# Performance work log

Measured on AMD Instinct MI355X. Metric: run time of the kernel, lower is better.

Reference implementation:

```python
import jax, jax.numpy as jnp
import numpy as np

DIM_K = 128
MODEL_DIM = 1024
B, S = 8, 2048

def setup_inputs() -> dict:
    key = jax.random.key(0)
    k1, k2, k3, k4, k5, k6, k7 = jax.random.split(key, 7)
    return {
        "query": jax.random.normal(k1, (B, S, MODEL_DIM), dtype=jnp.float32),
        "key": jax.random.normal(k2, (B, S, MODEL_DIM), dtype=jnp.float32),
        "value": jax.random.normal(k3, (B, S, MODEL_DIM), dtype=jnp.float32),
        "mask": jax.random.randint(k4, (B, S, S), 0, 2, dtype=jnp.int32),
        # nn.Linear(model_dim, dim_k, bias=False): weight shape [dim_k, model_dim]
        "Wq": jax.random.normal(k5, (DIM_K, MODEL_DIM), dtype=jnp.float32) * (MODEL_DIM ** -0.5),
        "Wk": jax.random.normal(k6, (DIM_K, MODEL_DIM), dtype=jnp.float32) * (MODEL_DIM ** -0.5),
        "Wv": jax.random.normal(k7, (DIM_K, MODEL_DIM), dtype=jnp.float32) * (MODEL_DIM ** -0.5),
    }

def reference(query, key, value, mask, Wq, Wk, Wv):
    # projections: y = x @ W.T
    q = jnp.einsum('bsm,km->bsk', query, Wq)
    k = jnp.einsum('bsm,km->bsk', key, Wk)
    v = jnp.einsum('bsm,km->bsk', value, Wv)
    scale = 1.0 / jnp.sqrt(jnp.float32(DIM_K))
    pre_score = jnp.einsum('bqk,bsk->bqs', q, k) * scale  # [B,Sq,Sk]
    pre_score = jnp.where(mask == 0, jnp.float32(-1e9), pre_score)
    score = jax.nn.softmax(pre_score, axis=-1)
    return jnp.einsum('bqs,bsk->bqk', score, v)
```

## Files before the change

kernel.cpp:

```cpp
#include <hip/hip_runtime.h>
#include <hip/hip_bf16.h>

#define SEQ 2048
#define DMODEL 1024
#define DK 128

typedef __bf16 bf16x8 __attribute__((ext_vector_type(8)));
typedef float  f32x4  __attribute__((ext_vector_type(4)));

#define L2E 1.44269504088896340736f

#define WS_Q  786432
#define WS_K  2883584
#define WS_VT 4980736
#define WS_BF16_BYTES 14155776ull

__global__ __launch_bounds__(256) void wconv_kernel(
    const float* __restrict__ wq, const float* __restrict__ wk,
    const float* __restrict__ wv, __bf16* __restrict__ wpack)
{
    int i = blockIdx.x * 256 + threadIdx.x;
    int p = i >> 17;
    int j = i & 131071;
    const float* src = (p == 0) ? wq : ((p == 1) ? wk : wv);
    float f = src[j];
    if (p == 0) f *= 0.08838834764831845f;
    __bf16 h = (__bf16)f;
    __bf16 l = (__bf16)(f - (float)h);
    wpack[p * 262144 + j]          = h;
    wpack[p * 262144 + 131072 + j] = l;
}

__global__ __launch_bounds__(256) void proj_kernel(
    const float* __restrict__ xq, const float* __restrict__ xk,
    const float* __restrict__ xv, const __bf16* __restrict__ wpack,
    __bf16* __restrict__ qws, __bf16* __restrict__ kws, __bf16* __restrict__ vtws)
{
    const int p = blockIdx.y;
    const float* __restrict__ x = (p == 0) ? xq : ((p == 1) ? xk : xv);
    const __bf16* __restrict__ whi_g = wpack + p * 262144;
    const __bf16* __restrict__ wlo_g = whi_g + 131072;

    const int mtile = blockIdx.x;
    const int m0 = mtile << 6;
    const int t = threadIdx.x;
    const int wv_ = t >> 6;
    const int lane = t & 63;
    const int l15 = lane & 15, g = lane >> 4;

    __shared__ __align__(16) __bf16 smem[18432];
    __bf16* whl = smem;
    __bf16* wll = smem + 9216;

    f32x4 acc[8];
#pragma unroll
    for (int nt = 0; nt < 8; ++nt) acc[nt] = (f32x4){0.f, 0.f, 0.f, 0.f};

    for (int kk = 0; kk < 16; ++kk) {
        __syncthreads();
#pragma unroll
        for (int i = 0; i < 8; ++i) {
            int idx = i * 256 + t;
            int h = idx >> 10, rem = idx & 1023;
            int row = rem >> 3, ck = rem & 7;
            const __bf16* src = (h ? wlo_g : whi_g) + row * 1024 + kk * 64 + ck * 8;
            __bf16* dst = (h ? wll : whl) + row * 72 + ck * 8;
            *(bf16x8*)dst = *(const bf16x8*)src;
        }
        __syncthreads();

#pragma unroll
        for (int ks = 0; ks < 2; ++ks) {
            int row = m0 + wv_ * 16 + l15;
            int col = kk * 64 + ks * 32 + g * 8;
            const float* xp = x + (size_t)row * 1024 + col;
            f32x4 a0 = *(const f32x4*)xp;
            f32x4 a1 = *(const f32x4*)(xp + 4);
            bf16x8 ah;
#pragma unroll
            for (int j = 0; j < 4; ++j) {
                ah[j] = (__bf16)a0[j];
                ah[4 + j] = (__bf16)a1[j];
            }
#pragma unroll
            for (int nt = 0; nt < 8; ++nt) {
                const __bf16* bp = whl + (nt * 16 + l15) * 72 + ks * 32 + g * 8;
                bf16x8 bh = *(const bf16x8*)bp;
                bf16x8 bl = *(const bf16x8*)(bp + 9216);
                acc[nt] = __builtin_amdgcn_mfma_f32_16x16x32_bf16(ah, bh, acc[nt], 0, 0, 0);
                acc[nt] = __builtin_amdgcn_mfma_f32_16x16x32_bf16(ah, bl, acc[nt], 0, 0, 0);
            }
        }
    }

    __syncthreads();
    __bf16* olds = smem;
#pragma unroll
    for (int nt = 0; nt < 8; ++nt)
#pragma unroll
        for (int r = 0; r < 4; ++r) {
            int rowl = wv_ * 16 + g * 4 + r;
            int col = nt * 16 + l15;
            __bf16 v = (__bf16)acc[nt][r];
            if (p < 2) olds[rowl * 136 + col] = v;
            else       olds[col * 72 + rowl] = v;
        }
    __syncthreads();

    const int bq = mtile >> 5, s0 = (mtile & 31) << 6;
    if (p < 2) {
#pragma unroll
        for (int i = 0; i < 4; ++i) {
            int idx = i * 256 + t;
            int row = idx >> 4, ck = idx & 15;
            bf16x8 v = *(const bf16x8*)(olds + row * 136 + ck * 8);
            __bf16* dst = ((p == 0) ? qws : kws) + (size_t)(m0 + row) * 128 + ck * 8;
            *(bf16x8*)dst = v;
        }
    } else {
#pragma unroll
        for (int i = 0; i < 4; ++i) {
            int idx = i * 256 + t;
            int row = idx >> 3, ck = idx & 7;
            bf16x8 v = *(const bf16x8*)(olds + row * 72 + ck * 8);
            __bf16* dst = vtws + ((size_t)(bq * 128 + row)) * 2048 + s0 + ck * 8;
            *(bf16x8*)dst = v;
        }
    }
}

__global__ __launch_bounds__(256) void flash_kernel(
    const __bf16* __restrict__ qws, const __bf16* __restrict__ kws,
    const __bf16* __restrict__ vtws, const int* __restrict__ mask,
    float* __restrict__ out, float* __restrict__ part, float* __restrict__ mlbuf,
    int ktp)
{
    const int bb = blockIdx.x & 7;
    const int rest = blockIdx.x >> 3;
    const int mtile = rest & 31;
    const int jsplit = rest >> 5;
    const int sq0 = mtile << 6;
    const int t = threadIdx.x;
    const int wv_ = t >> 6;
    const int lane = t & 63;
    const int l15 = lane & 15, g = lane >> 4;

    __shared__ __align__(16) __bf16 smem[22528];
    __bf16* klds = smem;
    __bf16* vtlds = smem + 8704;
    __bf16* plds = smem + 17920 + wv_ * 1152;

    bf16x8 qf[4];
    {
        const __bf16* qp = qws + ((size_t)(bb * 2048 + sq0 + wv_ * 16 + l15)) * 128 + g * 8;
#pragma unroll
        for (int ks = 0; ks < 4; ++ks) qf[ks] = *(const bf16x8*)(qp + ks * 32);
    }

    f32x4 o[8];
#pragma unroll
    for (int nt = 0; nt < 8; ++nt) o[nt] = (f32x4){0.f, 0.f, 0.f, 0.f};
    float m_run[4], l_run[4];
#pragma unroll
    for (int r = 0; r < 4; ++r) { m_run[r] = -__builtin_inff(); l_run[r] = 0.f; }

    const int* mbase = mask + ((size_t)(bb * 2048 + sq0 + wv_ * 16 + g * 4)) * 2048 + l15;

    const int kt_begin = jsplit * ktp, kt_end = kt_begin + ktp;
    for (int kt = kt_begin; kt < kt_end; ++kt) {
        const int n0 = kt << 6;
        __syncthreads();
#pragma unroll
        for (int i = 0; i < 8; ++i) {
            int idx = i * 256 + t;
            if (idx < 1024) {
                int row = idx >> 4, ck = idx & 15;
                *(bf16x8*)(klds + row * 136 + ck * 8) =
                    *(const bf16x8*)(kws + ((size_t)(bb * 2048 + n0 + row)) * 128 + ck * 8);
            } else {
                int v = idx - 1024;
                int row = v >> 3, ck = v & 7;
                *(bf16x8*)(vtlds + row * 72 + ck * 8) =
                    *(const bf16x8*)(vtws + ((size_t)(bb * 128 + row)) * 2048 + n0 + ck * 8);
            }
        }
        __syncthreads();

        int mv[4][4];
#pragma unroll
        for (int nt = 0; nt < 4; ++nt)
#pragma unroll
            for (int r = 0; r < 4; ++r)
                mv[nt][r] = mbase[(size_t)r * 2048 + n0 + nt * 16];

        f32x4 sf[4];
#pragma unroll
        for (int nt = 0; nt < 4; ++nt) sf[nt] = (f32x4){0.f, 0.f, 0.f, 0.f};
#pragma unroll
        for (int nt = 0; nt < 4; ++nt) {
            const __bf16* kp = klds + (nt * 16 + l15) * 136 + g * 8;
#pragma unroll
            for (int ks = 0; ks < 4; ++ks) {
                bf16x8 bfk = *(const bf16x8*)(kp + ks * 32);
                sf[nt] = __builtin_amdgcn_mfma_f32_16x16x32_bf16(qf[ks], bfk, sf[nt], 0, 0, 0);
            }
        }

        float mx[4], mnew[4], alpha[4], psum[4];
#pragma unroll
        for (int r = 0; r < 4; ++r)
            mx[r] = fmaxf(fmaxf(sf[0][r], sf[1][r]), fmaxf(sf[2][r], sf[3][r]));
#pragma unroll
        for (int off = 1; off < 16; off <<= 1)
#pragma unroll
            for (int r = 0; r < 4; ++r)
                mx[r] = fmaxf(mx[r], __shfl_xor(mx[r], off, 64));
#pragma unroll
        for (int r = 0; r < 4; ++r) {
            mnew[r] = fmaxf(m_run[r], mx[r]);
            alpha[r] = exp2f((m_run[r] - mnew[r]) * L2E);
            psum[r] = 0.f;
        }
#pragma unroll
        for (int nt = 0; nt < 4; ++nt)
#pragma unroll
            for (int r = 0; r < 4; ++r) {
                float pv = exp2f((sf[nt][r] - mnew[r]) * L2E);
                pv = mv[nt][r] ? pv : 0.f;
                psum[r] += pv;
                plds[(g * 4 + r) * 72 + nt * 16 + l15] = (__bf16)pv;
            }
#pragma unroll
        for (int off = 1; off < 16; off <<= 1)
#pragma unroll
            for (int r = 0; r < 4; ++r)
                psum[r] += __shfl_xor(psum[r], off, 64);
#pragma unroll
        for (int r = 0; r < 4; ++r) {
            l_run[r] = l_run[r] * alpha[r] + psum[r];
            m_run[r] = mnew[r];
        }
#pragma unroll
        for (int nt = 0; nt < 8; ++nt)
#pragma unroll
            for (int r = 0; r < 4; ++r) o[nt][r] *= alpha[r];

        bf16x8 pa[2];
#pragma unroll
        for (int ks2 = 0; ks2 < 2; ++ks2)
            pa[ks2] = *(const bf16x8*)(plds + l15 * 72 + ks2 * 32 + g * 8);

#pragma unroll
        for (int nt2 = 0; nt2 < 8; ++nt2) {
            const __bf16* vp = vtlds + (nt2 * 16 + l15) * 72 + g * 8;
#pragma unroll
            for (int ks2 = 0; ks2 < 2; ++ks2) {
                bf16x8 bfv = *(const bf16x8*)(vp + ks2 * 32);
                o[nt2] = __builtin_amdgcn_mfma_f32_16x16x32_bf16(pa[ks2], bfv, o[nt2], 0, 0, 0);
            }
        }
    }

    if (part == nullptr) {
        float inv[4];
#pragma unroll
        for (int r = 0; r < 4; ++r) inv[r] = 1.0f / l_run[r];
#pragma unroll
        for (int nt2 = 0; nt2 < 8; ++nt2)
#pragma unroll
            for (int r = 0; r < 4; ++r)
                out[((size_t)(bb * 2048 + sq0 + wv_ * 16 + g * 4 + r)) * 128 + nt2 * 16 + l15] =
                    o[nt2][r] * inv[r];
    } else {
#pragma unroll
        for (int nt2 = 0; nt2 < 8; ++nt2)
#pragma unroll
            for (int r = 0; r < 4; ++r) {
                size_t rowg = (size_t)(bb * 2048 + sq0 + wv_ * 16 + g * 4 + r);
                part[((size_t)jsplit * 16384 + rowg) * 128 + nt2 * 16 + l15] = o[nt2][r];
            }
        if (l15 == 0) {
#pragma unroll
            for (int r = 0; r < 4; ++r) {
                size_t rowg = (size_t)(bb * 2048 + sq0 + wv_ * 16 + g * 4 + r);
                mlbuf[((size_t)jsplit * 16384 + rowg) * 2]     = m_run[r];
                mlbuf[((size_t)jsplit * 16384 + rowg) * 2 + 1] = l_run[r];
            }
        }
    }
}

__global__ __launch_bounds__(256) void merge_kernel(
    const float* __restrict__ part, const float* __restrict__ mlbuf,
    float* __restrict__ out, int J)
{
    int t = threadIdx.x;
    size_t row = (size_t)blockIdx.x * 8 + (t >> 5);
    int c = (t & 31) * 4;
    float mj[4];
    float m = -__builtin_inff();
    for (int j = 0; j < J; ++j) {
        mj[j] = mlbuf[((size_t)j * 16384 + row) * 2];
        m = fmaxf(m, mj[j]);
    }
    float l = 0.f;
    f32x4 acc = (f32x4){0.f, 0.f, 0.f, 0.f};
    for (int j = 0; j < J; ++j) {
        float w = exp2f((mj[j] - m) * L2E);
        l += w * mlbuf[((size_t)j * 16384 + row) * 2 + 1];
        f32x4 v = *(const f32x4*)(part + ((size_t)j * 16384 + row) * 128 + c);
#pragma unroll
        for (int e = 0; e < 4; ++e) acc[e] += w * v[e];
    }
    float inv = 1.0f / l;
#pragma unroll
    for (int e = 0; e < 4; ++e) acc[e] *= inv;
    *(f32x4*)(out + row * 128 + c) = acc;
}

extern "C" void kernel_launch(void* const* d_in, const int* in_sizes, int n_in,
                              void* d_out, int out_size, void* d_ws, size_t ws_size,
                              hipStream_t stream)
{
    const float* query = (const float*)d_in[0];
    const float* key   = (const float*)d_in[1];
    const float* value = (const float*)d_in[2];
    const int*   mask  = (const int*)d_in[3];
    const float* Wq    = (const float*)d_in[4];
    const float* Wk    = (const float*)d_in[5];
    const float* Wv    = (const float*)d_in[6];
    float* out = (float*)d_out;

    __bf16* wpack = (__bf16*)d_ws;
    __bf16* qws = wpack + WS_Q;
    __bf16* kws = wpack + WS_K;
    __bf16* vtws = wpack + WS_VT;

    const size_t per_split = 16384ull * 128 * 4 + 16384ull * 8;
    int J = 1;
    if (ws_size >= WS_BF16_BYTES + 4 * per_split)      J = 4;
    else if (ws_size >= WS_BF16_BYTES + 2 * per_split) J = 2;
    float* part = (J > 1) ? (float*)((char*)d_ws + WS_BF16_BYTES) : nullptr;
    float* mlbuf = (J > 1) ? (part + (size_t)J * 16384 * 128) : nullptr;

    wconv_kernel<<<1536, 256, 0, stream>>>(Wq, Wk, Wv, wpack);
    proj_kernel<<<dim3(256, 3), 256, 0, stream>>>(query, key, value, wpack, qws, kws, vtws);
    flash_kernel<<<256 * J, 256, 0, stream>>>(qws, kws, vtws, mask, out, part, mlbuf, 32 / J);
    if (J > 1) merge_kernel<<<2048, 256, 0, stream>>>(part, mlbuf, out, J);
}
```

Baseline: 413.5 us.

## Switch to fp16 and restructure projection to read weights directly without LDS

Replaces bf16 with fp16 across the pipeline. This drops the hi/lo split-weight trick and halves the projection MFMAs. The projection kernel now uses 128 threads, each wave computing 32 rows, and reads fp16 weights straight from global/L2 instead of staging them through LDS with barriers. This removes the redundant second MFMA pass and the per-k-step synchronisation. The risk is fp16 range and precision limits on projected activations, plus higher global traffic for the weight reads.

```diff
diff --git a/kernel.cpp b/kernel.cpp
--- a/kernel.cpp
+++ b/kernel.cpp
@@ -1,23 +1,23 @@
 #include <hip/hip_runtime.h>
-#include <hip/hip_bf16.h>
+#include <hip/hip_fp16.h>
 
 #define SEQ 2048
 #define DMODEL 1024
 #define DK 128
 
-typedef __bf16 bf16x8 __attribute__((ext_vector_type(8)));
-typedef float  f32x4  __attribute__((ext_vector_type(4)));
+typedef _Float16 f16x8 __attribute__((ext_vector_type(8)));
+typedef float    f32x4 __attribute__((ext_vector_type(4)));
 
 #define L2E 1.44269504088896340736f
 
-#define WS_Q  786432
-#define WS_K  2883584
-#define WS_VT 4980736
-#define WS_BF16_BYTES 14155776ull
+#define WS_Q  393216
+#define WS_K  2490368
+#define WS_VT 4587520
+#define WS_F16_BYTES 13369344ull
 
 __global__ __launch_bounds__(256) void wconv_kernel(
     const float* __restrict__ wq, const float* __restrict__ wk,
-    const float* __restrict__ wv, __bf16* __restrict__ wpack)
+    const float* __restrict__ wv, _Float16* __restrict__ w16)
 {
     int i = blockIdx.x * 256 + threadIdx.x;
     int p = i >> 17;
@@ -25,21 +25,17 @@
     const float* src = (p == 0) ? wq : ((p == 1) ? wk : wv);
     float f = src[j];
     if (p == 0) f *= 0.08838834764831845f;
-    __bf16 h = (__bf16)f;
-    __bf16 l = (__bf16)(f - (float)h);
-    wpack[p * 262144 + j]          = h;
-    wpack[p * 262144 + 131072 + j] = l;
-}
-
-__global__ __launch_bounds__(256) void proj_kernel(
+    w16[i] = (_Float16)f;
+}
+
+__global__ __launch_bounds__(128) void proj_kernel(
     const float* __restrict__ xq, const float* __restrict__ xk,
-    const float* __restrict__ xv, const __bf16* __restrict__ wpack,
-    __bf16* __restrict__ qws, __bf16* __restrict__ kws, __bf16* __restrict__ vtws)
+    const float* __restrict__ xv, const _Float16* __restrict__ w16,
+    _Float16* __restrict__ qws, _Float16* __restrict__ kws, _Float16* __restrict__ vtws)
 {
     const int p = blockIdx.y;
     const float* __restrict__ x = (p == 0) ? xq : ((p == 1) ? xk : xv);
-    const __bf16* __restrict__ whi_g = wpack + p * 262144;
-    const __bf16* __restrict__ wlo_g = whi_g + 131072;
+    const _Float16* __restrict__ w = w16 + p * 131072;
 
     const int mtile = blockIdx.x;
     const int m0 = mtile << 6;
@@ -47,91 +43,81 @@
     const int wv_ = t >> 6;
     const int lane = t & 63;
     const int l15 = lane & 15, g = lane >> 4;
-
-    __shared__ __align__(16) __bf16 smem[18432];
-    __bf16* whl = smem;
-    __bf16* wll = smem + 9216;
-
-    f32x4 acc[8];
-#pragma unroll
-    for (int nt = 0; nt < 8; ++nt) acc[nt] = (f32x4){0.f, 0.f, 0.f, 0.f};
-
-    for (int kk = 0; kk < 16; ++kk) {
-        __syncthreads();
+    const int mw = m0 + wv_ * 32;
+
+    f32x4 acc[2][8];
+#pragma unroll
+    for (int mi = 0; mi < 2; ++mi)
+#pragma unroll
+        for (int nt = 0; nt < 8; ++nt) acc[mi][nt] = (f32x4){0.f, 0.f, 0.f, 0.f};
+
+    const float* x0 = x + (size_t)(mw + l15) * 1024 + g * 8;
+    const float* x1 = x0 + 16 * 1024;
+    const _Float16* wb = w + (size_t)l15 * 1024 + g * 8;
+
+#pragma unroll 2
+    for (int ks = 0; ks < 32; ++ks) {
+        const int col = ks * 32;
+        f32x4 a00 = *(const f32x4*)(x0 + col);
+        f32x4 a01 = *(const f32x4*)(x0 + col + 4);
+        f32x4 a10 = *(const f32x4*)(x1 + col);
+        f32x4 a11 = *(const f32x4*)(x1 + col + 4);
+        f16x8 af0, af1;
+#pragma unroll
+        for (int j = 0; j < 4; ++j) {
+            af0[j]     = (_Float16)a00[j];
+            af0[4 + j] = (_Float16)a01[j];
+            af1[j]     = (_Float16)a10[j];
+            af1[4 + j] = (_Float16)a11[j];
+        }
+#pragma unroll
+        for (int nt = 0; nt < 8; ++nt) {
+            f16x8 bf = *(const f16x8*)(wb + (size_t)nt * 16 * 1024 + col);
+            acc[0][nt] = __builtin_amdgcn_mfma_f32_16x16x32_f16(af0, bf, acc[0][nt], 0, 0, 0);
+            acc[1][nt] = __builtin_amdgcn_mfma_f32_16x16x32_f16(af1, bf, acc[1][nt], 0, 0, 0);
+        }
+    }
+
+    __shared__ __align__(16) _Float16 olds[9216];
+#pragma unroll
+    for (int mi = 0; mi < 2; ++mi)
+#pragma unroll
+        for (int nt = 0; nt < 8; ++nt)
+#pragma unroll
+            for (int r = 0; r < 4; ++r) {
+                int rowl = wv_ * 32 + mi * 16 + g * 4 + r;
+                int col = nt * 16 + l15;
+                _Float16 v = (_Float16)acc[mi][nt][r];
+                if (p < 2) olds[rowl * 136 + col] = v;
+                else       olds[col * 72 + rowl] = v;
+            }
+    __syncthreads();
+
+    if (p < 2) {
 #pragma unroll
         for (int i = 0; i < 8; ++i) {
-            int idx = i * 256 + t;
-            int h = idx >> 10, rem = idx & 1023;
-            int row = rem >> 3, ck = rem & 7;
-            const __bf16* src = (h ? wlo_g : whi_g) + row * 1024 + kk * 64 + ck * 8;
-            __bf16* dst = (h ? wll : whl) + row * 72 + ck * 8;
-            *(bf16x8*)dst = *(const bf16x8*)src;
-        }
-        __syncthreads();
-
-#pragma unroll
-        for (int ks = 0; ks < 2; ++ks) {
-            int row = m0 + wv_ * 16 + l15;
-            int col = kk * 64 + ks * 32 + g * 8;
-            const float* xp = x + (size_t)row * 1024 + col;
-            f32x4 a0 = *(const f32x4*)xp;
-            f32x4 a1 = *(const f32x4*)(xp + 4);
-            bf16x8 ah;
-#pragma unroll
-            for (int j = 0; j < 4; ++j) {
-                ah[j] = (__bf16)a0[j];
-                ah[4 + j] = (__bf16)a1[j];
-            }
-#pragma unroll
-            for (int nt = 0; nt < 8; ++nt) {
-                const __bf16* bp = whl + (nt * 16 + l15) * 72 + ks * 32 + g * 8;
-                bf16x8 bh = *(const bf16x8*)bp;
-                bf16x8 bl = *(const bf16x8*)(bp + 9216);
-                acc[nt] = __builtin_amdgcn_mfma_f32_16x16x32_bf16(ah, bh, acc[nt], 0, 0, 0);
-                acc[nt] = __builtin_amdgcn_mfma_f32_16x16x32_bf16(ah, bl, acc[nt], 0, 0, 0);
-            }
-        }
-    }
-
-    __syncthreads();
-    __bf16* olds = smem;
-#pragma unroll
-    for (int nt = 0; nt < 8; ++nt)
-#pragma unroll
-        for (int r = 0; r < 4; ++r) {
-            int rowl = wv_ * 16 + g * 4 + r;
-            int col = nt * 16 + l15;
-            __bf16 v = (__bf16)acc[nt][r];
-            if (p < 2) olds[rowl * 136 + col] = v;
-            else       olds[col * 72 + rowl] = v;
-        }
-    __syncthreads();
-
-    const int bq = mtile >> 5, s0 = (mtile & 31) << 6;
-    if (p < 2) {
-#pragma unroll
-        for (int i = 0; i < 4; ++i) {
-            int idx = i * 256 + t;
+            int idx = i * 128 + t;
             int row = idx >> 4, ck = idx & 15;
-            bf16x8 v = *(const bf16x8*)(olds + row * 136 + ck * 8);
-            __bf16* dst = ((p == 0) ? qws : kws) + (size_t)(m0 + row) * 128 + ck * 8;
-            *(bf16x8*)dst = v;
+            f16x8 v = *(const f16x8*)(olds + row * 136 + ck * 8);
+            _Float16* dst = ((p == 0) ? qws : kws) + (size_t)(m0 + row) * 128 + ck * 8;
+            *(f16x8*)dst = v;
         }
     } else {
-#pragma unroll
-        for (int i = 0; i < 4; ++i) {
-            int idx = i * 256 + t;
+        const int bq = mtile >> 5, s0 = (mtile & 31) << 6;
+#pragma unroll
+        for (int i = 0; i < 8; ++i) {
+            int idx = i * 128 + t;
             int row = idx >> 3, ck = idx & 7;
-            bf16x8 v = *(const bf16x8*)(olds + row * 72 + ck * 8);
-            __bf16* dst = vtws + ((size_t)(bq * 128 + row)) * 2048 + s0 + ck * 8;
-            *(bf16x8*)dst = v;
+            f16x8 v = *(const f16x8*)(olds + row * 72 + ck * 8);
+            _Float16* dst = vtws + ((size_t)(bq * 128 + row)) * 2048 + s0 + ck * 8;
+            *(f16x8*)dst = v;
         }
     }
 }
 
 __global__ __launch_bounds__(256) void flash_kernel(
-    const __bf16* __restrict__ qws, const __bf16* __restrict__ kws,
-    const __bf16* __restrict__ vtws, const int* __restrict__ mask,
+    const _Float16* __restrict__ qws, const _Float16* __restrict__ kws,
+    const _Float16* __restrict__ vtws, const int* __restrict__ mask,
     float* __restrict__ out, float* __restrict__ part, float* __restrict__ mlbuf,
     int ktp)
 {
@@ -145,16 +131,16 @@
     const int lane = t & 63;
     const int l15 = lane & 15, g = lane >> 4;
 
-    __shared__ __align__(16) __bf16 smem[22528];
-    __bf16* klds = smem;
-    __bf16* vtlds = smem + 8704;
-    __bf16* plds = smem + 17920 + wv_ * 1152;
-
-    bf16x8 qf[4];
+    __shared__ __align__(16) _Float16 smem[22528];
+    _Float16* klds = smem;
+    _Float16* vtlds = smem + 8704;
+    _Float16* plds = smem + 17920 + wv_ * 1152;
+
+    f16x8 qf[4];
     {
-        const __bf16* qp = qws + ((size_t)(bb * 2048 + sq0 + wv_ * 16 + l15)) * 128 + g * 8;
-#pragma unroll
-        for (int ks = 0; ks < 4; ++ks) qf[ks] = *(const bf16x8*)(qp + ks * 32);
+        const _Float16* qp = qws + ((size_t)(bb * 2048 + sq0 + wv_ * 16 + l15)) * 128 + g * 8;
+#pragma unroll
+        for (int ks = 0; ks < 4; ++ks) qf[ks] = *(const f16x8*)(qp + ks * 32);
     }
 
     f32x4 o[8];
@@ -175,13 +161,13 @@
             int idx = i * 256 + t;
             if (idx < 1024) {
                 int row = idx >> 4, ck = idx & 15;
-                *(bf16x8*)(klds + row * 136 + ck * 8) =
-                    *(const bf16x8*)(kws + ((size_t)(bb * 2048 + n0 + row)) * 128 + ck * 8);
+                *(f16x8*)(klds + row * 136 + ck * 8) =
+                    *(const f16x8*)(kws + ((size_t)(bb * 2048 + n0 + row)) * 128 + ck * 8);
             } else {
                 int v = idx - 1024;
                 int row = v >> 3, ck = v & 7;
-                *(bf16x8*)(vtlds + row * 72 + ck * 8) =
-                    *(const bf16x8*)(vtws + ((size_t)(bb * 128 + row)) * 2048 + n0 + ck * 8);
+                *(f16x8*)(vtlds + row * 72 + ck * 8) =
+                    *(const f16x8*)(vtws + ((size_t)(bb * 128 + row)) * 2048 + n0 + ck * 8);
             }
         }
         __syncthreads();
@@ -198,11 +184,11 @@
         for (int nt = 0; nt < 4; ++nt) sf[nt] = (f32x4){0.f, 0.f, 0.f, 0.f};
 #pragma unroll
         for (int nt = 0; nt < 4; ++nt) {
-            const __bf16* kp = klds + (nt * 16 + l15) * 136 + g * 8;
+            const _Float16* kp = klds + (nt * 16 + l15) * 136 + g * 8;
 #pragma unroll
             for (int ks = 0; ks < 4; ++ks) {
-                bf16x8 bfk = *(const bf16x8*)(kp + ks * 32);
-                sf[nt] = __builtin_amdgcn_mfma_f32_16x16x32_bf16(qf[ks], bfk, sf[nt], 0, 0, 0);
+                f16x8 bfk = *(const f16x8*)(kp + ks * 32);
+                sf[nt] = __builtin_amdgcn_mfma_f32_16x16x32_f16(qf[ks], bfk, sf[nt], 0, 0, 0);
             }
         }
 
@@ -228,7 +214,7 @@
                 float pv = exp2f((sf[nt][r] - mnew[r]) * L2E);
                 pv = mv[nt][r] ? pv : 0.f;
                 psum[r] += pv;
-                plds[(g * 4 + r) * 72 + nt * 16 + l15] = (__bf16)pv;
+                plds[(g * 4 + r) * 72 + nt * 16 + l15] = (_Float16)pv;
             }
 #pragma unroll
         for (int off = 1; off < 16; off <<= 1)
@@ -245,18 +231,18 @@
 #pragma unroll
             for (int r = 0; r < 4; ++r) o[nt][r] *= alpha[r];
 
-        bf16x8 pa[2];
+        f16x8 pa[2];
 #pragma unroll
         for (int ks2 = 0; ks2 < 2; ++ks2)
-            pa[ks2] = *(const bf16x8*)(plds + l15 * 72 + ks2 * 32 + g * 8);
+            pa[ks2] = *(const f16x8*)(plds + l15 * 72 + ks2 * 32 + g * 8);
 
 #pragma unroll
         for (int nt2 = 0; nt2 < 8; ++nt2) {
-            const __bf16* vp = vtlds + (nt2 * 16 + l15) * 72 + g * 8;
+            const _Float16* vp = vtlds + (nt2 * 16 + l15) * 72 + g * 8;
 #pragma unroll
             for (int ks2 = 0; ks2 < 2; ++ks2) {
-                bf16x8 bfv = *(const bf16x8*)(vp + ks2 * 32);
-                o[nt2] = __builtin_amdgcn_mfma_f32_16x16x32_bf16(pa[ks2], bfv, o[nt2], 0, 0, 0);
+                f16x8 bfv = *(const f16x8*)(vp + ks2 * 32);
+                o[nt2] = __builtin_amdgcn_mfma_f32_16x16x32_f16(pa[ks2], bfv, o[nt2], 0, 0, 0);
             }
         }
     }
@@ -331,20 +317,20 @@
     const float* Wv    = (const float*)d_in[6];
     float* out = (float*)d_out;
 
-    __bf16* wpack = (__bf16*)d_ws;
-    __bf16* qws = wpack + WS_Q;
-    __bf16* kws = wpack + WS_K;
-    __bf16* vtws = wpack + WS_VT;
+    _Float16* w16 = (_Float16*)d_ws;
+    _Float16* qws = w16 + WS_Q;
+    _Float16* kws = w16 + WS_K;
+    _Float16* vtws = w16 + WS_VT;
 
     const size_t per_split = 16384ull * 128 * 4 + 16384ull * 8;
     int J = 1;
-    if (ws_size >= WS_BF16_BYTES + 4 * per_split)      J = 4;
-    else if (ws_size >= WS_BF16_BYTES + 2 * per_split) J = 2;
-    float* part = (J > 1) ? (float*)((char*)d_ws + WS_BF16_BYTES) : nullptr;
+    if (ws_size >= WS_F16_BYTES + 4 * per_split)      J = 4;
+    else if (ws_size >= WS_F16_BYTES + 2 * per_split) J = 2;
+    float* part = (J > 1) ? (float*)((char*)d_ws + WS_F16_BYTES) : nullptr;
     float* mlbuf = (J > 1) ? (part + (size_t)J * 16384 * 128) : nullptr;
 
-    wconv_kernel<<<1536, 256, 0, stream>>>(Wq, Wk, Wv, wpack);
-    proj_kernel<<<dim3(256, 3), 256, 0, stream>>>(query, key, value, wpack, qws, kws, vtws);
+    wconv_kernel<<<1536, 256, 0, stream>>>(Wq, Wk, Wv, w16);
+    proj_kernel<<<dim3(256, 3), 128, 0, stream>>>(query, key, value, w16, qws, kws, vtws);
     flash_kernel<<<256 * J, 256, 0, stream>>>(qws, kws, vtws, mask, out, part, mlbuf, 32 / J);
     if (J > 1) merge_kernel<<<2048, 256, 0, stream>>>(part, mlbuf, out, J);
 }
```

New measurement: 395.8 us. -4.3%, faster.
